# Kernel optimization log

Measured on AMD Instinct MI355X. Metric: run time of the kernel, lower is better.

Reference implementation:

```python
import jax, jax.numpy as jnp
import numpy as np

N, E, FIN, H, G, L = 100000, 300000, 128, 256, 4000, 5
BN_EPS = 1e-5

def setup_inputs() -> dict:
    key = jax.random.key(0)
    ks = jax.random.split(key, 24)
    s = 0.05
    inp = {
        "x": jax.random.normal(ks[0], (N, FIN), dtype=jnp.float32),
        "edge_index": jax.random.randint(ks[1], (2, E), 0, N, dtype=jnp.int64),
        "batch": jnp.sort(jax.random.randint(ks[2], (N,), 0, G, dtype=jnp.int64)),
        # input projection
        "in_W": jax.random.normal(ks[3], (FIN, H), dtype=jnp.float32) * s,
        "in_b": jnp.zeros((H,), dtype=jnp.float32),
        # stacked per-layer GIN MLP params (Linear-BN-ReLU-Linear-BN-ReLU)
        "conv_W1": jax.random.normal(ks[4], (L, H, H), dtype=jnp.float32) * s,
        "conv_b1": jnp.zeros((L, H), dtype=jnp.float32),
        "conv_g1": jnp.ones((L, H), dtype=jnp.float32),
        "conv_be1": jnp.zeros((L, H), dtype=jnp.float32),
        "conv_W2": jax.random.normal(ks[5], (L, H, H), dtype=jnp.float32) * s,
        "conv_b2": jnp.zeros((L, H), dtype=jnp.float32),
        "conv_g2": jnp.ones((L, H), dtype=jnp.float32),
        "conv_be2": jnp.zeros((L, H), dtype=jnp.float32),
        "eps": jnp.zeros((L,), dtype=jnp.float32),
        # head MLP
        "head_W1": jax.random.normal(ks[6], (H, H // 2), dtype=jnp.float32) * s,
        "head_b1": jnp.zeros((H // 2,), dtype=jnp.float32),
        "head_W2": jax.random.normal(ks[7], (H // 2, 1), dtype=jnp.float32) * s,
        "head_b2": jnp.zeros((1,), dtype=jnp.float32),
    }
    return inp

def _bn(h, g, b):
    # BatchNorm1d over node dim (training-mode batch stats)
    m = jnp.mean(h, axis=0)
    v = jnp.var(h, axis=0)
    return g * (h - m) * jax.lax.rsqrt(v + BN_EPS) + b

def reference(x, edge_index, batch, in_W, in_b, conv_W1, conv_b1, conv_g1,
              conv_be1, conv_W2, conv_b2, conv_g2, conv_be2, eps,
              head_W1, head_b1, head_W2, head_b2):
    src, dst = edge_index[0], edge_index[1]
    h = jax.nn.relu(x @ in_W + in_b)  # [N,H]
    for l in range(L):
        agg = jax.ops.segment_sum(h[src], dst, num_segments=N)  # scatter-add
        z = (1.0 + eps[l]) * h + agg
        z = jax.nn.relu(_bn(z @ conv_W1[l] + conv_b1[l], conv_g1[l], conv_be1[l]))
        h = jax.nn.relu(_bn(z @ conv_W2[l] + conv_b2[l], conv_g2[l], conv_be2[l]))
        # dropout is identity in eval/reference
    # global mean pool by graph id
    sums = jax.ops.segment_sum(h, batch, num_segments=G)  # [G,H]
    cnt = jax.ops.segment_sum(jnp.ones((N,), h.dtype), batch, num_segments=G)
    pooled = sums / jnp.maximum(cnt, 1.0)[:, None]
    hid = jax.nn.relu(pooled @ head_W1 + head_b1)
    return hid @ head_W2 + head_b2  # [G,1]
```

## Files before the change

### kernel.cpp

```cpp
#include <hip/hip_runtime.h>
#include <hip/hip_bf16.h>
#include <stdint.h>
#include <stddef.h>

#define NN 100000
#define NE 300000
#define FINDIM 128
#define HD 256
#define NG 4000
#define NLAYER 5
#define MPAD 100096
#define NT (MPAD/32)
#define MG 384

typedef __attribute__((ext_vector_type(8))) short bf8;
typedef __attribute__((ext_vector_type(4))) float f4;

#define FENCE() __asm__ volatile("" ::: "memory")
#define WAITVM2() __asm__ volatile("s_waitcnt vmcnt(2)" ::: "memory")
#define WAITVM4() __asm__ volatile("s_waitcnt vmcnt(4)" ::: "memory")
#define WAITVM6() __asm__ volatile("s_waitcnt vmcnt(6)" ::: "memory")
#define WAITLGKM() __asm__ volatile("s_waitcnt lgkmcnt(0)" ::: "memory")
#define BARRIER() do { FENCE(); __builtin_amdgcn_s_barrier(); FENCE(); } while(0)

__device__ __forceinline__ unsigned short f2bf(float f){
  union { float f; unsigned u; } uf; uf.f = f;
  unsigned r = uf.u + 0x7fffu + ((uf.u >> 16) & 1u);
  return (unsigned short)(r >> 16);
}
__device__ __forceinline__ float bf2f(unsigned short h){
  union { unsigned u; float f; } uf; uf.u = ((unsigned)h) << 16; return uf.f;
}

__device__ __forceinline__ void gload16(const void* g, void* l){
  __builtin_amdgcn_global_load_lds((const __attribute__((address_space(1))) void*)g,
                                   (__attribute__((address_space(3))) void*)l, 16, 0, 0);
}

__global__ void k_zero(int* __restrict__ p, int n){
  int i = blockIdx.x*256 + threadIdx.x;
  if(i < n) p[i] = 0;
}

__global__ void k_count(const int* __restrict__ ei, int* __restrict__ counts){
  int e = blockIdx.x*256 + threadIdx.x;
  if(e < NE) atomicAdd(&counts[ei[NE + e]], 1);
}

__global__ void k_scan_partial(const int* __restrict__ counts, int* __restrict__ partials){
  __shared__ int sw[4];
  int b = blockIdx.x, t = threadIdx.x;
  int base = b*1024 + t*4;
  int s = 0;
  #pragma unroll
  for(int j=0;j<4;j++){ int i = base+j; if(i < NN) s += counts[i]; }
  #pragma unroll
  for(int d=1; d<64; d<<=1) s += __shfl_xor(s, d, 64);
  if((t & 63) == 0) sw[t>>6] = s;
  __syncthreads();
  if(t == 0) partials[b] = sw[0]+sw[1]+sw[2]+sw[3];
}

__global__ void k_scan_tot(int* __restrict__ partials, int* __restrict__ offsets, int nb){
  __shared__ int sm[128];
  int t = threadIdx.x;
  int v = (t < nb) ? partials[t] : 0;
  sm[t] = v; __syncthreads();
  for(int d=1; d<128; d<<=1){
    int x = 0;
    if(t >= d) x = sm[t-d];
    __syncthreads();
    sm[t] += x;
    __syncthreads();
  }
  if(t < nb) partials[t] = sm[t] - v;
  if(t == 127) offsets[NN] = sm[127];
}

__global__ void k_scan_final(const int* __restrict__ counts, const int* __restrict__ partials,
                             int* __restrict__ offsets, int* __restrict__ cursor){
  __shared__ int wsum[4];
  int b = blockIdx.x, t = threadIdx.x;
  int base = b*1024 + t*4;
  int c[4]; int ts = 0;
  #pragma unroll
  for(int j=0;j<4;j++){ int i = base+j; c[j] = (i < NN) ? counts[i] : 0; ts += c[j]; }
  int lane = t & 63;
  int inc = ts;
  #pragma unroll
  for(int d=1; d<64; d<<=1){ int x = __shfl_up(inc, d, 64); if(lane >= d) inc += x; }
  if(lane == 63) wsum[t>>6] = inc;
  __syncthreads();
  int woff = 0;
  for(int w2=0; w2<(t>>6); w2++) woff += wsum[w2];
  int excl = partials[b] + woff + inc - ts;
  #pragma unroll
  for(int j=0;j<4;j++){
    int i = base+j;
    if(i < NN){ offsets[i] = excl; cursor[i] = excl; excl += c[j]; }
  }
}

__global__ void k_fill(const int* __restrict__ ei, int* __restrict__ cursor, int* __restrict__ eidx){
  int e = blockIdx.x*256 + threadIdx.x;
  if(e < NE){
    int d = ei[NE + e];
    int pos = atomicAdd(&cursor[d], 1);
    eidx[pos] = ei[e];
  }
}

__global__ void k_wt(const float* __restrict__ src, unsigned short* __restrict__ dst, int K, int Ncols){
  int l = blockIdx.y;
  size_t base = (size_t)l * K * Ncols;
  int i = blockIdx.x*256 + threadIdx.x;
  if(i < K*Ncols){
    int k = i / Ncols, n = i % Ncols;
    dst[base + (size_t)n*K + k] = f2bf(src[base + i]);
  }
}

template<int TRANS, bool RELUOUT, bool STATS>
__global__ __launch_bounds__(256, 3) void k_gemmb(
    const unsigned short* __restrict__ A, const unsigned short* __restrict__ Bt,
    const float* __restrict__ bias, const float* __restrict__ preS,
    const float* __restrict__ preT, unsigned short* __restrict__ C,
    float* __restrict__ stats)
{
  __shared__ __align__(16) unsigned short As[3][8192];
  __shared__ __align__(16) unsigned short Cs[4][576];
  const int t = threadIdx.x;
  const int lane = t & 63, w = t >> 6;
  const int q = lane >> 4, ln = lane & 15;
  const int nh = blockIdx.x & 1;
  const int mg = blockIdx.x >> 1;
  const int nbase = nh*128 + w*32;

  bf8 bb[2][8];
  #pragma unroll
  for(int nf=0; nf<2; nf++)
    #pragma unroll
    for(int s=0; s<8; s++)
      bb[nf][s] = *(const bf8*)(Bt + (size_t)(nbase + nf*16 + ln)*HD + s*32 + q*8);

  float bv[2];
  #pragma unroll
  for(int nf=0; nf<2; nf++) bv[nf] = bias[nbase + nf*16 + ln];

  f4 sA = (f4){0.f,0.f,0.f,0.f}, sB = sA, tA = sA, tB = sA;
  if(TRANS){
    int cc = (t & 31) * 8;
    sA = *(const f4*)(preS + cc);  sB = *(const f4*)(preS + cc + 4);
    tA = *(const f4*)(preT + cc);  tB = *(const f4*)(preT + cc + 4);
  }

  auto issueA = [&](int mt, int b){
    const int m0 = mt*32;
    #pragma unroll
    for(int j=0; j<4; j++){
      int slot = j*256 + t;
      int row = slot >> 5, p = slot & 31;
      int c = p ^ (row & 7);
      gload16(A + (size_t)(m0 + row)*HD + c*8, &As[b][(j*256 + w*64)*8]);
    }
  };

  float sacc[2] = {0.f, 0.f}, ssacc[2] = {0.f, 0.f};

  issueA(mg, 0);
  issueA(mg + MG, 1);

  int k = 0;
  for(int mt = mg; mt < NT; mt += MG, k++){
    const bool last = (mt + MG >= NT);
    if(last)        WAITVM2();
    else if(k == 0) WAITVM4();
    else            WAITVM6();
    BARRIER();

    unsigned short* Ab = &As[k % 3][0];
    const int m0 = mt*32;
    const bool padt = (m0 >= NN);

    if(padt){
      uint4 z = (uint4){0u,0u,0u,0u};
      int r2 = lane >> 2, sg = lane & 3;
      *(uint4*)&C[(size_t)(m0 + r2)*HD + nbase + sg*8]      = z;
      *(uint4*)&C[(size_t)(m0 + 16 + r2)*HD + nbase + sg*8] = z;
    } else {
      if(TRANS){
        const int r0 = t >> 5;
        const int p  = (t & 31) ^ r0;
        #pragma unroll
        for(int i=0; i<4; i++){
          int row = r0 + 8*i;
          uint4 u = *(uint4*)&Ab[(row*32 + p)*8];
          unsigned short* us = (unsigned short*)&u;
          #pragma unroll
          for(int e=0; e<8; e++){
            float sc = (e<4) ? sA[e] : sB[e-4];
            float sh = (e<4) ? tA[e] : tB[e-4];
            float v = bf2f(us[e]);
            v = fmaxf(fmaf(sc, v, sh), 0.f);
            us[e] = f2bf(v);
          }
          *(uint4*)&Ab[(row*32 + p)*8] = u;
        }
        WAITLGKM();
        BARRIER();
      }

      f4 acc[2][2];
      #pragma unroll
      for(int i=0;i<2;i++)
        #pragma unroll
        for(int j=0;j<2;j++) acc[i][j] = (f4){0.f,0.f,0.f,0.f};

      __builtin_amdgcn_s_setprio(1);
      #pragma unroll
      for(int s=0; s<8; s++){
        bf8 af[2];
        #pragma unroll
        for(int mi=0; mi<2; mi++){
          int row = mi*16 + ln;
          int p = (s*4 + q) ^ (row & 7);
          af[mi] = *(const bf8*)&Ab[row*256 + p*8];
        }
        #pragma unroll
        for(int mi=0; mi<2; mi++)
          #pragma unroll
          for(int nf=0; nf<2; nf++)
            acc[mi][nf] = __builtin_amdgcn_mfma_f32_16x16x32_bf16(af[mi], bb[nf][s], acc[mi][nf], 0, 0, 0);
      }
      __builtin_amdgcn_s_setprio(0);

      if(STATS){
        #pragma unroll
        for(int nf=0; nf<2; nf++)
          #pragma unroll
          for(int mi=0; mi<2; mi++)
            #pragma unroll
            for(int r=0; r<4; r++){
              float v = acc[mi][nf][r];
              sacc[nf] += v; ssacc[nf] = fmaf(v, v, ssacc[nf]);
            }
      }

      unsigned short* wsc = &Cs[w][0];
      #pragma unroll
      for(int mi=0; mi<2; mi++){
        #pragma unroll
        for(int nf=0; nf<2; nf++)
          #pragma unroll
          for(int r=0; r<4; r++){
            float v = acc[mi][nf][r] + bv[nf];
            if(RELUOUT) v = fmaxf(v, 0.f);
            wsc[(q*4 + r)*36 + nf*16 + ln] = f2bf(v);
          }
        int r2 = lane >> 2, sg = lane & 3;
        uint4 u = *(const uint4*)&wsc[r2*36 + sg*8];
        *(uint4*)&C[(size_t)(m0 + mi*16 + r2)*HD + nbase + sg*8] = u;
      }
    }

    FENCE();
    if(mt + 2*MG < NT) issueA(mt + 2*MG, (k+2) % 3);
  }

  if(STATS){
    #pragma unroll
    for(int nf=0; nf<2; nf++){
      float s = sacc[nf], ss = ssacc[nf];
      s  += __shfl_xor(s, 16, 64);  s  += __shfl_xor(s, 32, 64);
      ss += __shfl_xor(ss, 16, 64); ss += __shfl_xor(ss, 32, 64);
      if(q == 0){
        int gn = nbase + nf*16 + ln;
        atomicAdd(&stats[gn], s);
        atomicAdd(&stats[HD + gn], ss);
      }
    }
  }
}

__global__ __launch_bounds__(256, 3) void k_gemmb_in(
    const float* __restrict__ A, const unsigned short* __restrict__ Bt,
    const float* __restrict__ bias, unsigned short* __restrict__ C)
{
  __shared__ __align__(16) unsigned short As[4096];
  __shared__ __align__(16) unsigned short Cs[4][1152];
  const int t = threadIdx.x;
  const int lane = t & 63, w = t >> 6;
  const int q = lane >> 4, ln = lane & 15;
  const int nh = blockIdx.x & 1;
  const int mg = blockIdx.x >> 1;
  const int nbase = nh*128 + w*32;

  bf8 bb[2][4];
  #pragma unroll
  for(int nf=0; nf<2; nf++)
    #pragma unroll
    for(int s=0; s<4; s++)
      bb[nf][s] = *(const bf8*)(Bt + (size_t)(nbase + nf*16 + ln)*FINDIM + s*32 + q*8);

  float bv[2];
  #pragma unroll
  for(int nf=0; nf<2; nf++) bv[nf] = bias[nbase + nf*16 + ln];

  for(int mt = mg; mt < NT; mt += MG){
    const int m0 = mt*32;
    const bool padt = (m0 >= NN);
    __syncthreads();
    #pragma unroll
    for(int j=0; j<2; j++){
      int slot = j*256 + t;
      int row = slot >> 4, p = slot & 15;
      int c = p ^ (row & 7);
      int gm = m0 + row;
      f4 v0 = (f4){0.f,0.f,0.f,0.f}, v1 = (f4){0.f,0.f,0.f,0.f};
      if(gm < NN){
        v0 = *(const f4*)&A[(size_t)gm*FINDIM + c*8];
        v1 = *(const f4*)&A[(size_t)gm*FINDIM + c*8 + 4];
      }
      ushort4 a0, a1;
      a0.x = f2bf(v0.x); a0.y = f2bf(v0.y); a0.z = f2bf(v0.z); a0.w = f2bf(v0.w);
      a1.x = f2bf(v1.x); a1.y = f2bf(v1.y); a1.z = f2bf(v1.z); a1.w = f2bf(v1.w);
      *(ushort4*)&As[row*128 + p*8]     = a0;
      *(ushort4*)&As[row*128 + p*8 + 4] = a1;
    }
    __syncthreads();

    f4 acc[2][2];
    #pragma unroll
    for(int i=0;i<2;i++)
      #pragma unroll
      for(int j=0;j<2;j++) acc[i][j] = (f4){0.f,0.f,0.f,0.f};

    #pragma unroll
    for(int s=0; s<4; s++){
      bf8 af[2];
      #pragma unroll
      for(int mi=0; mi<2; mi++){
        int row = mi*16 + ln;
        int p = (s*4 + q) ^ (row & 7);
        af[mi] = *(const bf8*)&As[row*128 + p*8];
      }
      #pragma unroll
      for(int mi=0; mi<2; mi++)
        #pragma unroll
        for(int nf=0; nf<2; nf++)
          acc[mi][nf] = __builtin_amdgcn_mfma_f32_16x16x32_bf16(af[mi], bb[nf][s], acc[mi][nf], 0, 0, 0);
    }

    unsigned short* wsc = &Cs[w][0];
    #pragma unroll
    for(int mi=0; mi<2; mi++)
      #pragma unroll
      for(int nf=0; nf<2; nf++)
        #pragma unroll
        for(int r=0; r<4; r++){
          float v = fmaxf(acc[mi][nf][r] + bv[nf], 0.f);
          if(padt) v = 0.f;
          wsc[(mi*16 + q*4 + r)*36 + nf*16 + ln] = f2bf(v);
        }
    int r2 = lane >> 1, ch = lane & 1;
    size_t cb = (size_t)(m0 + r2)*HD + nh*128 + w*32;
    uint4 u0 = *(const uint4*)&wsc[r2*36 + ch*8];
    uint4 u1 = *(const uint4*)&wsc[r2*36 + (ch+2)*8];
    *(uint4*)&C[cb + ch*8]     = u0;
    *(uint4*)&C[cb + (ch+2)*8] = u1;
  }
}

__global__ void k_bnfin(const float* __restrict__ cs, const float* __restrict__ bias,
                        const float* __restrict__ g, const float* __restrict__ be,
                        float* __restrict__ sc, float* __restrict__ sh){
  int c = threadIdx.x;
  float m0 = cs[c] * (1.0f/NN);
  float mean = m0 + bias[c];
  float var  = cs[HD + c] * (1.0f/NN) - m0*m0;
  float s = g[c] * rsqrtf(var + 1e-5f);
  sc[c] = s;
  sh[c] = be[c] - mean*s;
}

__device__ __forceinline__ void acc8(f4& alo, f4& ahi, uint4 u, float wt,
                                     f4 s0, f4 s1, f4 t0, f4 t1, int ident){
  const unsigned short* us = (const unsigned short*)&u;
  float v[8];
  #pragma unroll
  for(int e=0;e<8;e++) v[e] = bf2f(us[e]);
  if(!ident){
    v[0] = fmaxf(fmaf(s0.x, v[0], t0.x), 0.f);
    v[1] = fmaxf(fmaf(s0.y, v[1], t0.y), 0.f);
    v[2] = fmaxf(fmaf(s0.z, v[2], t0.z), 0.f);
    v[3] = fmaxf(fmaf(s0.w, v[3], t0.w), 0.f);
    v[4] = fmaxf(fmaf(s1.x, v[4], t1.x), 0.f);
    v[5] = fmaxf(fmaf(s1.y, v[5], t1.y), 0.f);
    v[6] = fmaxf(fmaf(s1.z, v[6], t1.z), 0.f);
    v[7] = fmaxf(fmaf(s1.w, v[7], t1.w), 0.f);
  }
  alo.x = fmaf(wt, v[0], alo.x); alo.y = fmaf(wt, v[1], alo.y);
  alo.z = fmaf(wt, v[2], alo.z); alo.w = fmaf(wt, v[3], alo.w);
  ahi.x = fmaf(wt, v[4], ahi.x); ahi.y = fmaf(wt, v[5], ahi.y);
  ahi.z = fmaf(wt, v[6], ahi.z); ahi.w = fmaf(wt, v[7], ahi.w);
}

__global__ __launch_bounds__(256) void k_agg(const unsigned short* __restrict__ src,
    unsigned short* __restrict__ dst,
    const int* __restrict__ offs, const int* __restrict__ eidx,
    const float* __restrict__ eps, int l,
    const float* __restrict__ sc, const float* __restrict__ sh, int ident)
{
  int wv = threadIdx.x >> 6;
  int n = blockIdx.x*4 + wv;
  if(n >= NN) return;
  int lane = threadIdx.x & 63;
  int h = lane >> 5, l5 = lane & 31;
  int c = l5 * 8;

  f4 s0=(f4){0.f,0.f,0.f,0.f}, s1=s0, t0=s0, t1=s0;
  if(!ident){
    s0 = *(const f4*)(sc + c); s1 = *(const f4*)(sc + c + 4);
    t0 = *(const f4*)(sh + c); t1 = *(const f4*)(sh + c + 4);
  }
  float ep = 1.f + eps[l];

  f4 alo = (f4){0.f,0.f,0.f,0.f}, ahi = alo;
  int lo = offs[n], hi = offs[n+1];

  bool first = true;
  for(int base = lo; first || base < hi; base += 64){
    int cnt = hi - base; if(cnt > 64) cnt = 64; if(cnt < 0) cnt = 0;
    int R = cnt + (first ? 1 : 0);
    int idx = (base + lane < hi) ? eidx[base + lane] : 0;
    for(int r0 = 0; r0 < R; r0 += 4){
      int my0 = r0 + h, my1 = r0 + 2 + h;
      bool v0 = my0 < R, v1 = my1 < R;
      bool self0 = first && (my0 == 0);
      int j0 = (first ? my0 - 1 : my0) & 63;
      int j1 = (first ? my1 - 1 : my1) & 63;
      int sr0 = __shfl(idx, j0, 64);
      int sr1 = __shfl(idx, j1, 64);
      int row0 = self0 ? n : sr0;
      float w0 = self0 ? ep : 1.f;
      uint4 u0, u1;
      if(v0) u0 = *(const uint4*)(src + (size_t)row0*HD + c);
      if(v1) u1 = *(const uint4*)(src + (size_t)sr1*HD + c);
      if(v0) acc8(alo, ahi, u0, w0, s0, s1, t0, t1, ident);
      if(v1) acc8(alo, ahi, u1, 1.f, s0, s1, t0, t1, ident);
    }
    first = false;
  }

  #pragma unroll
  for(int e=0;e<4;e++){
    alo[e] += __shfl_xor(alo[e], 32, 64);
    ahi[e] += __shfl_xor(ahi[e], 32, 64);
  }
  if(h == 0){
    unsigned short o[8];
    o[0]=f2bf(alo.x); o[1]=f2bf(alo.y); o[2]=f2bf(alo.z); o[3]=f2bf(alo.w);
    o[4]=f2bf(ahi.x); o[5]=f2bf(ahi.y); o[6]=f2bf(ahi.z); o[7]=f2bf(ahi.w);
    *(uint4*)(dst + (size_t)n*HD + c) = *(const uint4*)o;
  }
}

__device__ __forceinline__ int lowb(const int* __restrict__ arr, int n, int key){
  int lo = 0, hi = n;
  while(lo < hi){ int mid = (lo + hi) >> 1; if(arr[mid] < key) lo = mid + 1; else hi = mid; }
  return lo;
}

__global__ __launch_bounds__(256) void k_pool(const unsigned short* __restrict__ src,
    const int* __restrict__ batch,
    const float* __restrict__ sc, const float* __restrict__ sh, float* __restrict__ pooled)
{
  int wv = threadIdx.x >> 6;
  int g = blockIdx.x*4 + wv;
  if(g >= NG) return;
  int lane = threadIdx.x & 63;
  int c = lane << 2;
  int lo = lowb(batch, NN, g);
  int hi = lowb(batch, NN, g+1);
  f4 s4 = *(const f4*)(sc + c);
  f4 t4 = *(const f4*)(sh + c);
  f4 acc = (f4){0.f,0.f,0.f,0.f};
  for(int n=lo; n<hi; n++){
    ushort4 uv = *(const ushort4*)(src + (size_t)n*HD + c);
    acc.x += fmaxf(fmaf(s4.x, bf2f(uv.x), t4.x), 0.f);
    acc.y += fmaxf(fmaf(s4.y, bf2f(uv.y), t4.y), 0.f);
    acc.z += fmaxf(fmaf(s4.z, bf2f(uv.z), t4.z), 0.f);
    acc.w += fmaxf(fmaf(s4.w, bf2f(uv.w), t4.w), 0.f);
  }
  float inv = 1.0f / fmaxf((float)(hi - lo), 1.0f);
  acc.x *= inv; acc.y *= inv; acc.z *= inv; acc.w *= inv;
  *(f4*)(pooled + (size_t)g*HD + c) = acc;
}

__global__ __launch_bounds__(128) void k_head(const float* __restrict__ pooled,
    const float* __restrict__ W1, const float* __restrict__ b1,
    const float* __restrict__ W2, const float* __restrict__ b2, float* __restrict__ out)
{
  __shared__ float p[HD];
  __shared__ float red[2];
  int g = blockIdx.x, t = threadIdx.x;
  if(t < 64) *(f4*)&p[t*4] = *(const f4*)(pooled + (size_t)g*HD + t*4);
  __syncthreads();
  float s = b1[t];
  for(int k=0;k<HD;k++) s = fmaf(p[k], W1[k*128 + t], s);
  float o = fmaxf(s, 0.f) * W2[t];
  #pragma unroll
  for(int d=1; d<64; d<<=1) o += __shfl_xor(o, d, 64);
  if((t & 63) == 0) red[t>>6] = o;
  __syncthreads();
  if(t == 0) out[g] = red[0] + red[1] + b2[0];
}

extern "C" void kernel_launch(void* const* d_in, const int* in_sizes, int n_in,
                              void* d_out, int out_size, void* d_ws, size_t ws_size,
                              hipStream_t stream) {
  const float* x    = (const float*)d_in[0];
  const int*   ei   = (const int*)  d_in[1];
  const int*   bat  = (const int*)  d_in[2];
  const float* inW  = (const float*)d_in[3];
  const float* inb  = (const float*)d_in[4];
  const float* W1   = (const float*)d_in[5];
  const float* b1   = (const float*)d_in[6];
  const float* g1   = (const float*)d_in[7];
  const float* be1  = (const float*)d_in[8];
  const float* W2   = (const float*)d_in[9];
  const float* b2   = (const float*)d_in[10];
  const float* g2   = (const float*)d_in[11];
  const float* be2  = (const float*)d_in[12];
  const float* eps  = (const float*)d_in[13];
  const float* hW1  = (const float*)d_in[14];
  const float* hb1  = (const float*)d_in[15];
  const float* hW2  = (const float*)d_in[16];
  const float* hb2  = (const float*)d_in[17];
  float* out = (float*)d_out;

  char* p = (char*)d_ws;
  auto alloc = [&](size_t bytes)->char*{
    char* r = p; p += (bytes + 255) & ~(size_t)255; return r;
  };
  unsigned short* B0 = (unsigned short*)alloc((size_t)MPAD*HD*2);
  unsigned short* B1 = (unsigned short*)alloc((size_t)MPAD*HD*2);
  unsigned short* Wtin = (unsigned short*)alloc((size_t)FINDIM*HD*2);
  unsigned short* Wt1  = (unsigned short*)alloc((size_t)NLAYER*HD*HD*2);
  unsigned short* Wt2  = (unsigned short*)alloc((size_t)NLAYER*HD*HD*2);
  int* counts  = (int*)alloc((size_t)NN*4);
  int* offsets = (int*)alloc((size_t)(NN+1)*4);
  int* cursor  = (int*)alloc((size_t)NN*4);
  int* eidx    = (int*)alloc((size_t)NE*4);
  int* partials= (int*)alloc(128*4);
  float* cs    = (float*)alloc(4*HD*4);
  float* bnp   = (float*)alloc(4*HD*4);
  float* pooled= (float*)alloc((size_t)NG*HD*4);

  k_zero<<<(NN+255)/256, 256, 0, stream>>>(counts, NN);
  k_count<<<(NE+255)/256, 256, 0, stream>>>(ei, counts);
  int nb = (NN + 1023)/1024;
  k_scan_partial<<<nb, 256, 0, stream>>>(counts, partials);
  k_scan_tot<<<1, 128, 0, stream>>>(partials, offsets, nb);
  k_scan_final<<<nb, 256, 0, stream>>>(counts, partials, offsets, cursor);
  k_fill<<<(NE+255)/256, 256, 0, stream>>>(ei, cursor, eidx);

  k_wt<<<dim3((FINDIM*HD+255)/256, 1), 256, 0, stream>>>(inW, Wtin, FINDIM, HD);
  k_wt<<<dim3((HD*HD+255)/256, NLAYER), 256, 0, stream>>>(W1, Wt1, HD, HD);
  k_wt<<<dim3((HD*HD+255)/256, NLAYER), 256, 0, stream>>>(W2, Wt2, HD, HD);

  {
    int padInts = (MPAD - NN) * HD / 2;
    k_zero<<<(padInts+255)/256, 256, 0, stream>>>((int*)(B1 + (size_t)NN*HD), padInts);
  }

  k_gemmb_in<<<2*MG, 256, 0, stream>>>(x, Wtin, inb, B0);

  float* sc1 = bnp, *sh1 = bnp + HD, *sc2 = bnp + 2*HD, *sh2 = bnp + 3*HD;
  unsigned short* hbuf = B0;
  unsigned short* tbuf = B1;
  for(int l=0; l<NLAYER; l++){
    k_zero<<<4, 256, 0, stream>>>((int*)cs, 4*HD);
    k_agg<<<(NN+3)/4, 256, 0, stream>>>(hbuf, tbuf, offsets, eidx, eps, l, sc2, sh2, l==0 ? 1 : 0);
    k_gemmb<0, false, true><<<2*MG, 256, 0, stream>>>(tbuf, Wt1 + (size_t)l*HD*HD, b1 + l*HD,
                                                      nullptr, nullptr, hbuf, cs);
    k_bnfin<<<1, HD, 0, stream>>>(cs, b1 + l*HD, g1 + l*HD, be1 + l*HD, sc1, sh1);
    k_gemmb<1, false, true><<<2*MG, 256, 0, stream>>>(hbuf, Wt2 + (size_t)l*HD*HD, b2 + l*HD,
                                                      sc1, sh1, tbuf, cs + 2*HD);
    k_bnfin<<<1, HD, 0, stream>>>(cs + 2*HD, b2 + l*HD, g2 + l*HD, be2 + l*HD, sc2, sh2);
    unsigned short* tmp = hbuf; hbuf = tbuf; tbuf = tmp;
  }

  k_pool<<<(NG+3)/4, 256, 0, stream>>>(hbuf, bat, sc2, sh2, pooled);
  k_head<<<NG, 128, 0, stream>>>(pooled, hW1, hb1, hW2, hb2, out);
}
```

Measured before the change: 800.1 us.

## Stage GEMM A tiles through registers and use packed FMA in aggregation

The GEMM no longer uses direct global-to-LDS loads with a triple buffer. It prefetches the next-next A tile into registers after the MFMA loop, then stores it into a double-buffered LDS slot before a barrier each iteration. Separately, the aggregation kernel unpacks bf16 pairs and applies the BN affine and accumulation with v_pk_fma_f32 to halve the FMA instruction count. The register staging raises VGPR pressure, which could hurt occupancy at 3 blocks per CU, and it adds a barrier per tile.

New measurement: 1.038 ms. 29.7% more time.

```diff
diff --git a/kernel.cpp b/kernel.cpp
--- a/kernel.cpp
+++ b/kernel.cpp
@@ -15,11 +15,9 @@
 
 typedef __attribute__((ext_vector_type(8))) short bf8;
 typedef __attribute__((ext_vector_type(4))) float f4;
+typedef __attribute__((ext_vector_type(2))) float f2;
 
 #define FENCE() __asm__ volatile("" ::: "memory")
-#define WAITVM2() __asm__ volatile("s_waitcnt vmcnt(2)" ::: "memory")
-#define WAITVM4() __asm__ volatile("s_waitcnt vmcnt(4)" ::: "memory")
-#define WAITVM6() __asm__ volatile("s_waitcnt vmcnt(6)" ::: "memory")
 #define WAITLGKM() __asm__ volatile("s_waitcnt lgkmcnt(0)" ::: "memory")
 #define BARRIER() do { FENCE(); __builtin_amdgcn_s_barrier(); FENCE(); } while(0)
 
@@ -32,9 +30,15 @@
   union { unsigned u; float f; } uf; uf.u = ((unsigned)h) << 16; return uf.f;
 }
 
-__device__ __forceinline__ void gload16(const void* g, void* l){
-  __builtin_amdgcn_global_load_lds((const __attribute__((address_space(1))) void*)g,
-                                   (__attribute__((address_space(3))) void*)l, 16, 0, 0);
+__device__ __forceinline__ f2 pk_fma(f2 a, f2 b, f2 c){
+  f2 d;
+  asm("v_pk_fma_f32 %0, %1, %2, %3" : "=v"(d) : "v"(a), "v"(b), "v"(c));
+  return d;
+}
+__device__ __forceinline__ f2 up2(unsigned wd){
+  union { unsigned u; float f; } a, b;
+  a.u = wd << 16; b.u = wd & 0xffff0000u;
+  return (f2){a.f, b.f};
 }
 
 __global__ void k_zero(int* __restrict__ p, int n){
@@ -127,7 +131,7 @@
     const float* __restrict__ preT, unsigned short* __restrict__ C,
     float* __restrict__ stats)
 {
-  __shared__ __align__(16) unsigned short As[3][8192];
+  __shared__ __align__(16) unsigned short As[2][8192];
   __shared__ __align__(16) unsigned short Cs[4][576];
   const int t = threadIdx.x;
   const int lane = t & 63, w = t >> 6;
@@ -154,33 +158,37 @@
     tA = *(const f4*)(preT + cc);  tB = *(const f4*)(preT + cc + 4);
   }
 
-  auto issueA = [&](int mt, int b){
+  auto loadA = [&](int mt, uint4 (&rg)[4]){
     const int m0 = mt*32;
     #pragma unroll
     for(int j=0; j<4; j++){
-      int slot = j*256 + t;
-      int row = slot >> 5, p = slot & 31;
-      int c = p ^ (row & 7);
-      gload16(A + (size_t)(m0 + row)*HD + c*8, &As[b][(j*256 + w*64)*8]);
+      int row = j*8 + (t>>5);
+      int c = (t&31) ^ (row & 7);
+      rg[j] = *(const uint4*)(A + (size_t)(m0 + row)*HD + c*8);
     }
   };
+  auto storeA = [&](int b, uint4 (&rg)[4]){
+    #pragma unroll
+    for(int j=0; j<4; j++)
+      *(uint4*)&As[b][(j*256 + t)*8] = rg[j];
+  };
 
   float sacc[2] = {0.f, 0.f}, ssacc[2] = {0.f, 0.f};
 
-  issueA(mg, 0);
-  issueA(mg + MG, 1);
+  uint4 ra[4], rb[4];
+  loadA(mg, ra);
+  loadA(mg + MG, rb);
+  storeA(0, ra);
+  WAITLGKM();
+  BARRIER();
 
   int k = 0;
   for(int mt = mg; mt < NT; mt += MG, k++){
-    const bool last = (mt + MG >= NT);
-    if(last)        WAITVM2();
-    else if(k == 0) WAITVM4();
-    else            WAITVM6();
-    BARRIER();
-
-    unsigned short* Ab = &As[k % 3][0];
+    unsigned short* Ab = &As[k & 1][0];
     const int m0 = mt*32;
     const bool padt = (m0 >= NN);
+    const bool hn  = (mt + MG   < NT);
+    const bool hn2 = (mt + 2*MG < NT);
 
     if(padt){
       uint4 z = (uint4){0u,0u,0u,0u};
@@ -234,6 +242,11 @@
       }
       __builtin_amdgcn_s_setprio(0);
 
+      if(hn2){
+        if((k & 1) == 0) loadA(mt + 2*MG, ra);
+        else             loadA(mt + 2*MG, rb);
+      }
+
       if(STATS){
         #pragma unroll
         for(int nf=0; nf<2; nf++)
@@ -263,8 +276,17 @@
       }
     }
 
-    FENCE();
-    if(mt + 2*MG < NT) issueA(mt + 2*MG, (k+2) % 3);
+    if(padt && hn2){
+      if((k & 1) == 0) loadA(mt + 2*MG, ra);
+      else             loadA(mt + 2*MG, rb);
+    }
+
+    if(hn){
+      if((k & 1) == 0) storeA(1, rb);
+      else             storeA(0, ra);
+      WAITLGKM();
+    }
+    BARRIER();
   }
 
   if(STATS){
@@ -383,26 +405,19 @@
   sh[c] = be[c] - mean*s;
 }
 
-__device__ __forceinline__ void acc8(f4& alo, f4& ahi, uint4 u, float wt,
-                                     f4 s0, f4 s1, f4 t0, f4 t1, int ident){
-  const unsigned short* us = (const unsigned short*)&u;
-  float v[8];
-  #pragma unroll
-  for(int e=0;e<8;e++) v[e] = bf2f(us[e]);
-  if(!ident){
-    v[0] = fmaxf(fmaf(s0.x, v[0], t0.x), 0.f);
-    v[1] = fmaxf(fmaf(s0.y, v[1], t0.y), 0.f);
-    v[2] = fmaxf(fmaf(s0.z, v[2], t0.z), 0.f);
-    v[3] = fmaxf(fmaf(s0.w, v[3], t0.w), 0.f);
-    v[4] = fmaxf(fmaf(s1.x, v[4], t1.x), 0.f);
-    v[5] = fmaxf(fmaf(s1.y, v[5], t1.y), 0.f);
-    v[6] = fmaxf(fmaf(s1.z, v[6], t1.z), 0.f);
-    v[7] = fmaxf(fmaf(s1.w, v[7], t1.w), 0.f);
-  }
-  alo.x = fmaf(wt, v[0], alo.x); alo.y = fmaf(wt, v[1], alo.y);
-  alo.z = fmaf(wt, v[2], alo.z); alo.w = fmaf(wt, v[3], alo.w);
-  ahi.x = fmaf(wt, v[4], ahi.x); ahi.y = fmaf(wt, v[5], ahi.y);
-  ahi.z = fmaf(wt, v[6], ahi.z); ahi.w = fmaf(wt, v[7], ahi.w);
+__device__ __forceinline__ void acc8p(f2 (&ac)[4], uint4 u, f2 wt,
+                                      const f2 (&s)[4], const f2 (&sh)[4], int ident){
+  const unsigned* ws = (const unsigned*)&u;
+  #pragma unroll
+  for(int i=0;i<4;i++){
+    f2 v = up2(ws[i]);
+    if(!ident){
+      v = pk_fma(s[i], v, sh[i]);
+      v.x = fmaxf(v.x, 0.f);
+      v.y = fmaxf(v.y, 0.f);
+    }
+    ac[i] = pk_fma(wt, v, ac[i]);
+  }
 }
 
 __global__ __launch_bounds__(256) void k_agg(const unsigned short* __restrict__ src,
@@ -418,14 +433,20 @@
   int h = lane >> 5, l5 = lane & 31;
   int c = l5 * 8;
 
-  f4 s0=(f4){0.f,0.f,0.f,0.f}, s1=s0, t0=s0, t1=s0;
+  f2 s[4] = {(f2){0.f,0.f},(f2){0.f,0.f},(f2){0.f,0.f},(f2){0.f,0.f}};
+  f2 sf[4] = {(f2){0.f,0.f},(f2){0.f,0.f},(f2){0.f,0.f},(f2){0.f,0.f}};
   if(!ident){
-    s0 = *(const f4*)(sc + c); s1 = *(const f4*)(sc + c + 4);
-    t0 = *(const f4*)(sh + c); t1 = *(const f4*)(sh + c + 4);
+    #pragma unroll
+    for(int i=0;i<4;i++){
+      s[i]  = *(const f2*)(sc + c + 2*i);
+      sf[i] = *(const f2*)(sh + c + 2*i);
+    }
   }
   float ep = 1.f + eps[l];
-
-  f4 alo = (f4){0.f,0.f,0.f,0.f}, ahi = alo;
+  f2 epw = (f2){ep, ep};
+  f2 one = (f2){1.f, 1.f};
+
+  f2 ac[4] = {(f2){0.f,0.f},(f2){0.f,0.f},(f2){0.f,0.f},(f2){0.f,0.f}};
   int lo = offs[n], hi = offs[n+1];
 
   bool first = true;
@@ -442,25 +463,25 @@
       int sr0 = __shfl(idx, j0, 64);
       int sr1 = __shfl(idx, j1, 64);
       int row0 = self0 ? n : sr0;
-      float w0 = self0 ? ep : 1.f;
+      f2 w0 = self0 ? epw : one;
       uint4 u0, u1;
       if(v0) u0 = *(const uint4*)(src + (size_t)row0*HD + c);
       if(v1) u1 = *(const uint4*)(src + (size_t)sr1*HD + c);
-      if(v0) acc8(alo, ahi, u0, w0, s0, s1, t0, t1, ident);
-      if(v1) acc8(alo, ahi, u1, 1.f, s0, s1, t0, t1, ident);
+      if(v0) acc8p(ac, u0, w0, s, sf, ident);
+      if(v1) acc8p(ac, u1, one, s, sf, ident);
     }
     first = false;
   }
 
   #pragma unroll
-  for(int e=0;e<4;e++){
-    alo[e] += __shfl_xor(alo[e], 32, 64);
-    ahi[e] += __shfl_xor(ahi[e], 32, 64);
+  for(int i=0;i<4;i++){
+    ac[i].x += __shfl_xor(ac[i].x, 32, 64);
+    ac[i].y += __shfl_xor(ac[i].y, 32, 64);
   }
   if(h == 0){
     unsigned short o[8];
-    o[0]=f2bf(alo.x); o[1]=f2bf(alo.y); o[2]=f2bf(alo.z); o[3]=f2bf(alo.w);
-    o[4]=f2bf(ahi.x); o[5]=f2bf(ahi.y); o[6]=f2bf(ahi.z); o[7]=f2bf(ahi.w);
+    #pragma unroll
+    for(int i=0;i<4;i++){ o[2*i] = f2bf(ac[i].x); o[2*i+1] = f2bf(ac[i].y); }
     *(uint4*)(dst + (size_t)n*HD + c) = *(const uint4*)o;
   }
 }
```

## Fold BN finalize and stat zeroing into consumer kernels, drop pad zero launch

Applied to the files above, without the earlier changes.

Removes the separate BatchNorm finalize kernels and the per-layer stats-zeroing launch. Each consumer (aggregation, second GEMM, pooling) now computes scale and shift from the raw column statistics, and the buffer that must be cleared is zeroed by block 0 of a preceding kernel. The aim is to cut about three small launches per layer plus the padding-zero launch. The risks are redundant per-thread recomputation of the coefficients and ordering hazards from zeroing stats inside kernels, and dropping the pad zeroing may leave the B1 padding rows uninitialised.

Result: slower. 818.8 us (+2.3%).

```diff
diff --git a/kernel.cpp b/kernel.cpp
--- a/kernel.cpp
+++ b/kernel.cpp
@@ -35,6 +35,18 @@
 __device__ __forceinline__ void gload16(const void* g, void* l){
   __builtin_amdgcn_global_load_lds((const __attribute__((address_space(1))) void*)g,
                                    (__attribute__((address_space(3))) void*)l, 16, 0, 0);
+}
+
+__device__ __forceinline__ void bncoef(const float* __restrict__ st,
+                                       const float* __restrict__ bb,
+                                       const float* __restrict__ gg,
+                                       const float* __restrict__ be,
+                                       int ch, float& s, float& sh){
+  float m0 = st[ch] * (1.0f/NN);
+  float mean = m0 + bb[ch];
+  float var  = st[HD + ch] * (1.0f/NN) - m0*m0;
+  s  = gg[ch] * rsqrtf(var + 1e-5f);
+  sh = be[ch] - mean*s;
 }
 
 __global__ void k_zero(int* __restrict__ p, int n){
@@ -123,9 +135,10 @@
 template<int TRANS, bool RELUOUT, bool STATS>
 __global__ __launch_bounds__(256, 3) void k_gemmb(
     const unsigned short* __restrict__ A, const unsigned short* __restrict__ Bt,
-    const float* __restrict__ bias, const float* __restrict__ preS,
-    const float* __restrict__ preT, unsigned short* __restrict__ C,
-    float* __restrict__ stats)
+    const float* __restrict__ bias, const float* __restrict__ bstats,
+    const float* __restrict__ bnb, const float* __restrict__ bng,
+    const float* __restrict__ bnbe, unsigned short* __restrict__ C,
+    float* __restrict__ stats, float* __restrict__ zstats)
 {
   __shared__ __align__(16) unsigned short As[3][8192];
   __shared__ __align__(16) unsigned short Cs[4][576];
@@ -136,6 +149,8 @@
   const int mg = blockIdx.x >> 1;
   const int nbase = nh*128 + w*32;
 
+  if(zstats && blockIdx.x == 0){ zstats[t] = 0.f; zstats[256 + t] = 0.f; }
+
   bf8 bb[2][8];
   #pragma unroll
   for(int nf=0; nf<2; nf++)
@@ -150,8 +165,13 @@
   f4 sA = (f4){0.f,0.f,0.f,0.f}, sB = sA, tA = sA, tB = sA;
   if(TRANS){
     int cc = (t & 31) * 8;
-    sA = *(const f4*)(preS + cc);  sB = *(const f4*)(preS + cc + 4);
-    tA = *(const f4*)(preT + cc);  tB = *(const f4*)(preT + cc + 4);
+    #pragma unroll
+    for(int e=0; e<8; e++){
+      float sv, sh;
+      bncoef(bstats, bnb, bng, bnbe, cc + e, sv, sh);
+      if(e < 4){ sA[e] = sv; tA[e] = sh; }
+      else     { sB[e-4] = sv; tB[e-4] = sh; }
+    }
   }
 
   auto issueA = [&](int mt, int b){
@@ -371,18 +391,6 @@
   }
 }
 
-__global__ void k_bnfin(const float* __restrict__ cs, const float* __restrict__ bias,
-                        const float* __restrict__ g, const float* __restrict__ be,
-                        float* __restrict__ sc, float* __restrict__ sh){
-  int c = threadIdx.x;
-  float m0 = cs[c] * (1.0f/NN);
-  float mean = m0 + bias[c];
-  float var  = cs[HD + c] * (1.0f/NN) - m0*m0;
-  float s = g[c] * rsqrtf(var + 1e-5f);
-  sc[c] = s;
-  sh[c] = be[c] - mean*s;
-}
-
 __device__ __forceinline__ void acc8(f4& alo, f4& ahi, uint4 u, float wt,
                                      f4 s0, f4 s1, f4 t0, f4 t1, int ident){
   const unsigned short* us = (const unsigned short*)&u;
@@ -409,8 +417,12 @@
     unsigned short* __restrict__ dst,
     const int* __restrict__ offs, const int* __restrict__ eidx,
     const float* __restrict__ eps, int l,
-    const float* __restrict__ sc, const float* __restrict__ sh, int ident)
+    const float* __restrict__ bstats, const float* __restrict__ bnb,
+    const float* __restrict__ bng, const float* __restrict__ bnbe,
+    float* __restrict__ zstats, int ident)
 {
+  if(blockIdx.x == 0){ zstats[threadIdx.x] = 0.f; zstats[256 + threadIdx.x] = 0.f; }
+
   int wv = threadIdx.x >> 6;
   int n = blockIdx.x*4 + wv;
   if(n >= NN) return;
@@ -420,8 +432,13 @@
 
   f4 s0=(f4){0.f,0.f,0.f,0.f}, s1=s0, t0=s0, t1=s0;
   if(!ident){
-    s0 = *(const f4*)(sc + c); s1 = *(const f4*)(sc + c + 4);
-    t0 = *(const f4*)(sh + c); t1 = *(const f4*)(sh + c + 4);
+    #pragma unroll
+    for(int e=0; e<8; e++){
+      float sv, sh;
+      bncoef(bstats, bnb, bng, bnbe, c + e, sv, sh);
+      if(e < 4){ s0[e] = sv; t0[e] = sh; }
+      else     { s1[e-4] = sv; t1[e-4] = sh; }
+    }
   }
   float ep = 1.f + eps[l];
 
@@ -473,7 +490,9 @@
 
 __global__ __launch_bounds__(256) void k_pool(const unsigned short* __restrict__ src,
     const int* __restrict__ batch,
-    const float* __restrict__ sc, const float* __restrict__ sh, float* __restrict__ pooled)
+    const float* __restrict__ bstats, const float* __restrict__ bnb,
+    const float* __restrict__ bng, const float* __restrict__ bnbe,
+    float* __restrict__ pooled)
 {
   int wv = threadIdx.x >> 6;
   int g = blockIdx.x*4 + wv;
@@ -482,8 +501,13 @@
   int c = lane << 2;
   int lo = lowb(batch, NN, g);
   int hi = lowb(batch, NN, g+1);
-  f4 s4 = *(const f4*)(sc + c);
-  f4 t4 = *(const f4*)(sh + c);
+  f4 s4, t4;
+  #pragma unroll
+  for(int e=0; e<4; e++){
+    float sv, sh;
+    bncoef(bstats, bnb, bng, bnbe, c + e, sv, sh);
+    s4[e] = sv; t4[e] = sh;
+  }
   f4 acc = (f4){0.f,0.f,0.f,0.f};
   for(int n=lo; n<hi; n++){
     ushort4 uv = *(const ushort4*)(src + (size_t)n*HD + c);
@@ -554,8 +578,10 @@
   int* eidx    = (int*)alloc((size_t)NE*4);
   int* partials= (int*)alloc(128*4);
   float* cs    = (float*)alloc(4*HD*4);
-  float* bnp   = (float*)alloc(4*HD*4);
   float* pooled= (float*)alloc((size_t)NG*HD*4);
+
+  float* cs1 = cs;
+  float* cs2 = cs + 2*HD;
 
   k_zero<<<(NN+255)/256, 256, 0, stream>>>(counts, NN);
   k_count<<<(NE+255)/256, 256, 0, stream>>>(ei, counts);
@@ -569,28 +595,26 @@
   k_wt<<<dim3((HD*HD+255)/256, NLAYER), 256, 0, stream>>>(W1, Wt1, HD, HD);
   k_wt<<<dim3((HD*HD+255)/256, NLAYER), 256, 0, stream>>>(W2, Wt2, HD, HD);
 
-  {
-    int padInts = (MPAD - NN) * HD / 2;
-    k_zero<<<(padInts+255)/256, 256, 0, stream>>>((int*)(B1 + (size_t)NN*HD), padInts);
-  }
-
   k_gemmb_in<<<2*MG, 256, 0, stream>>>(x, Wtin, inb, B0);
 
-  float* sc1 = bnp, *sh1 = bnp + HD, *sc2 = bnp + 2*HD, *sh2 = bnp + 3*HD;
   unsigned short* hbuf = B0;
   unsigned short* tbuf = B1;
   for(int l=0; l<NLAYER; l++){
-    k_zero<<<4, 256, 0, stream>>>((int*)cs, 4*HD);
-    k_agg<<<(NN+3)/4, 256, 0, stream>>>(hbuf, tbuf, offsets, eidx, eps, l, sc2, sh2, l==0 ? 1 : 0);
+    const float* pb  = (l > 0) ? (b2  + (l-1)*HD) : b2;
+    const float* pg  = (l > 0) ? (g2  + (l-1)*HD) : g2;
+    const float* pbe = (l > 0) ? (be2 + (l-1)*HD) : be2;
+    k_agg<<<(NN+3)/4, 256, 0, stream>>>(hbuf, tbuf, offsets, eidx, eps, l,
+                                        cs2, pb, pg, pbe, cs1, l==0 ? 1 : 0);
     k_gemmb<0, false, true><<<2*MG, 256, 0, stream>>>(tbuf, Wt1 + (size_t)l*HD*HD, b1 + l*HD,
-                                                      nullptr, nullptr, hbuf, cs);
-    k_bnfin<<<1, HD, 0, stream>>>(cs, b1 + l*HD, g1 + l*HD, be1 + l*HD, sc1, sh1);
+                                                      nullptr, nullptr, nullptr, nullptr,
+                                                      hbuf, cs1, cs2);
     k_gemmb<1, false, true><<<2*MG, 256, 0, stream>>>(hbuf, Wt2 + (size_t)l*HD*HD, b2 + l*HD,
-                                                      sc1, sh1, tbuf, cs + 2*HD);
-    k_bnfin<<<1, HD, 0, stream>>>(cs + 2*HD, b2 + l*HD, g2 + l*HD, be2 + l*HD, sc2, sh2);
+                                                      cs1, b1 + l*HD, g1 + l*HD, be1 + l*HD,
+                                                      tbuf, cs2, nullptr);
     unsigned short* tmp = hbuf; hbuf = tbuf; tbuf = tmp;
   }
 
-  k_pool<<<(NG+3)/4, 256, 0, stream>>>(hbuf, bat, sc2, sh2, pooled);
+  k_pool<<<(NG+3)/4, 256, 0, stream>>>(hbuf, bat, cs2, b2 + (NLAYER-1)*HD,
+                                       g2 + (NLAYER-1)*HD, be2 + (NLAYER-1)*HD, pooled);
   k_head<<<NG, 128, 0, stream>>>(pooled, hW1, hb1, hW2, hb2, out);
 }
```
